# Optimization experiments

Measured on AMD Instinct MI355X. Metric: run time of the kernel, lower is better.

## Reference

```python
import jax, jax.numpy as jnp
import numpy as np

NEG = -1e9  # finite stand-in for -inf (avoids inf-inf NaNs, safe in fp32)


def setup_inputs() -> dict:
    T, V, Lmax, A = 2048, 8192, 8, 64
    rng = np.random.default_rng(0)
    seq = rng.integers(0, A, size=T).astype(np.int32)
    # first A pieces are the single codepoints -> every sequence is segmentable
    piece_lens = np.concatenate([
        np.ones(A, np.int32),
        rng.integers(1, Lmax + 1, size=V - A).astype(np.int32),
    ])
    pieces = rng.integers(0, A, size=(V, Lmax)).astype(np.int32)
    pieces[:A, 0] = np.arange(A)
    logits = rng.standard_normal(V).astype(np.float32)
    m = logits.max()
    log_probs = (logits - m - np.log(np.exp(logits - m).sum())).astype(np.float32)
    return {
        'seq': jnp.asarray(seq),
        'pieces': jnp.asarray(pieces),
        'piece_lens': jnp.asarray(piece_lens),
        'log_probs': jnp.asarray(log_probs),
    }


def reference(seq, pieces, piece_lens, log_probs):
    T = seq.shape[0]
    V, Lmax = pieces.shape
    dt = log_probs.dtype

    # --- match table: match[t, i] = piece i matches sequence at position t ---
    seq_pad = jnp.concatenate([seq, jnp.full((Lmax,), -1, seq.dtype)])
    windows = seq_pad[jnp.arange(T)[:, None] + jnp.arange(Lmax)[None, :]]  # [T, Lmax]
    lmask = jnp.arange(Lmax)[None, :] < piece_lens[:, None]                # [V, Lmax]
    eq = windows[:, None, :] == pieces[None, :, :]                        # [T, V, Lmax]
    fits = (jnp.arange(T)[:, None] + piece_lens[None, :]) <= T            # [T, V]
    match = jnp.all(eq | ~lmask[None, :, :], axis=-1) & fits              # [T, V]
    mlp = jnp.where(match, log_probs[None, :], NEG).astype(dt)            # [T, V]

    # end_logp[t-1, i] = mlp[t - len_i, i]  (piece i ending exactly at t, t=1..T)
    te = jnp.arange(1, T + 1)[:, None]
    src = te - piece_lens[None, :]
    end_logp = jnp.where(src >= 0,
                         mlp[jnp.clip(src, 0, T - 1), jnp.arange(V)[None, :]],
                         NEG)

    # --- forward pass: alpha[t] = logsumexp_i alpha[t - len_i] + log p_i ---
    idx_a = Lmax - piece_lens  # window slot holding alpha[t - len_i]
    def fstep(win, row):
        a_t = jax.nn.logsumexp(win[idx_a] + row)
        return jnp.concatenate([win[1:], a_t[None]]), a_t
    win0 = jnp.full((Lmax,), NEG, dt).at[-1].set(0.0)
    _, alpha_rest = jax.lax.scan(fstep, win0, end_logp)
    alpha = jnp.concatenate([jnp.zeros((1,), dt), alpha_rest])  # [T+1]

    # --- backward pass: beta[t] = logsumexp_i log p_i + beta[t + len_i] ---
    idx_b = piece_lens - 1  # window slot holding beta[t + len_i]
    def bstep(win, row):
        b_t = jax.nn.logsumexp(row + win[idx_b])
        return jnp.concatenate([b_t[None], win[:-1]]), b_t
    winT = jnp.full((Lmax,), NEG, dt).at[0].set(0.0)
    _, beta_rev = jax.lax.scan(bstep, winT, mlp[::-1])
    beta = jnp.concatenate([beta_rev[::-1], jnp.zeros((1,), dt)])  # [T+1]

    # --- posteriors: P[t, i] = exp(alpha[t] + log p_i + beta[t+len_i] - alpha[T]) ---
    norm = alpha[T]
    beta_next = beta[jnp.clip(jnp.arange(T)[:, None] + piece_lens[None, :], 0, T)]
    P = jnp.exp(alpha[:T][:, None] + mlp + beta_next - norm)
    P = jnp.where(match, P, 0.0)
    return jnp.where(norm > NEG / 2, P, jnp.zeros_like(P))
```

## Files before the change

### kernel.cpp

```cpp
#include <hip/hip_runtime.h>
#include <stdint.h>

#define LMAX 8
#define KCH 32
#define NC  64
#define TT  2048
#define LN2D 0.6931471805599453
#define NEGE (-(1<<28))

struct __align__(16) PK { unsigned long long key; float logp; int len; };

__device__ __forceinline__ int fexp(float m) { return ((__float_as_int(m) >> 23) & 0xFF) - 127; }
__device__ __forceinline__ int fexpbits(float m) { return (__float_as_int(m) >> 23) & 0xFF; }
__device__ __forceinline__ float p2(int e) { return __int_as_float((e + 127) << 23); }
__device__ __forceinline__ float p2c(int e) { return (e < -126) ? 0.f : p2(e); }

__global__ void k_prep(const int* __restrict__ seq, const int* __restrict__ pieces,
                       const int* __restrict__ plens, const float* __restrict__ logp,
                       PK* __restrict__ pk, unsigned long long* __restrict__ w64,
                       float* __restrict__ M, int T, int V) {
  int idx = blockIdx.x * blockDim.x + threadIdx.x;
  if (idx < V) {
    const int* pr = pieces + idx * LMAX;
    int len = plens[idx];
    unsigned long long key = 0ull;
    #pragma unroll
    for (int l = 0; l < LMAX; ++l) {
      unsigned long long b = (unsigned long long)(pr[l] & 0xFF);
      if (l < len) key |= b << (8 * l);
    }
    PK o; o.key = key; o.logp = logp[idx]; o.len = len;
    pk[idx] = o;
  } else if (idx < V + T) {
    int t = idx - V;
    unsigned long long w = 0ull;
    #pragma unroll
    for (int l = 0; l < LMAX; ++l) {
      int pos = t + l;
      unsigned long long b = (pos < T) ? (unsigned long long)(seq[pos] & 0xFF) : 0xFFull;
      w |= b << (8 * l);
    }
    w64[t] = w;
  } else if (idx < V + T + T * LMAX) {
    M[idx - V - T] = 0.f;
  }
}

__global__ void k_match(const PK* __restrict__ pk, const unsigned long long* __restrict__ w64,
                        float* __restrict__ M, int T, int V, int tPer) {
  int v = blockIdx.x * blockDim.x + threadIdx.x;
  PK p = pk[v];
  unsigned long long mask = (p.len >= 8) ? ~0ull : ((1ull << (8 * p.len)) - 1ull);
  unsigned long long key = p.key;
  int t0 = blockIdx.y * tPer;
  float prob = -1.f;
  for (int t = t0; t < t0 + tPer; ++t) {
    unsigned long long w = w64[t];
    if (((w ^ key) & mask) == 0ull) {
      if (prob < 0.f) prob = expf(p.logp);
      atomicAdd(&M[t * LMAX + (p.len - 1)], prob);
    }
  }
}

__global__ __launch_bounds__(64, 1) void k_chunks(const float* __restrict__ M,
        float* __restrict__ Wt, int* __restrict__ EWc) {
  int gtid = blockIdx.x * 64 + threadIdx.x;
  int task = gtid >> 3, b = gtid & 7;
  int dir = task >> 6, c = task & 63;
  int base = c * KCH;
  const float4* Mv = (const float4*)M;
  float v[8];
  #pragma unroll
  for (int i = 0; i < 8; ++i) v[i] = (i == b) ? 1.f : 0.f;
  int ec = 0;
  if (dir == 0) {
    float4 ra = Mv[base * 2], rb = Mv[base * 2 + 1];
    for (int kg = 0; kg < 4; ++kg) {
      #pragma unroll
      for (int kk = 0; kk < 8; ++kk) {
        int k = kg * 8 + kk;
        float4 c0 = ra, c1 = rb;
        int nk = (k + 1 < KCH) ? k + 1 : KCH - 1;
        ra = Mv[(base + nk) * 2]; rb = Mv[(base + nk) * 2 + 1];
        float a_ = v[kk & 7];
        v[(kk + 1) & 7] = fmaf(a_, c0.x, v[(kk + 1) & 7]);
        v[(kk + 2) & 7] = fmaf(a_, c0.y, v[(kk + 2) & 7]);
        v[(kk + 3) & 7] = fmaf(a_, c0.z, v[(kk + 3) & 7]);
        v[(kk + 4) & 7] = fmaf(a_, c0.w, v[(kk + 4) & 7]);
        v[(kk + 5) & 7] = fmaf(a_, c1.x, v[(kk + 5) & 7]);
        v[(kk + 6) & 7] = fmaf(a_, c1.y, v[(kk + 6) & 7]);
        v[(kk + 7) & 7] = fmaf(a_, c1.z, v[(kk + 7) & 7]);
        v[kk & 7]       = a_ * c1.w;
        if (kk == 3 || kk == 7) {
          float mx = 0.f;
          #pragma unroll
          for (int i = 0; i < 8; ++i) mx = fmaxf(mx, v[i]);
          if (fexpbits(mx) != 0) {
            int e = fexp(mx); float sc = p2(-e);
            #pragma unroll
            for (int i = 0; i < 8; ++i) v[i] *= sc;
            ec += e;
          }
        }
      }
    }
  } else {
    float4 ra = Mv[(base + KCH - 1) * 2], rb = Mv[(base + KCH - 1) * 2 + 1];
    for (int kg = 0; kg < 4; ++kg) {
      #pragma unroll
      for (int kk = 0; kk < 8; ++kk) {
        int k = kg * 8 + kk;
        float4 c0 = ra, c1 = rb;
        int nk = (k + 1 < KCH) ? k + 1 : KCH - 1;
        int nt = base + KCH - 1 - nk;
        ra = Mv[nt * 2]; rb = Mv[nt * 2 + 1];
        float nb =      c0.x * v[(8  - kk) & 7];
        nb = fmaf(c0.y, v[(9  - kk) & 7], nb);
        nb = fmaf(c0.z, v[(10 - kk) & 7], nb);
        nb = fmaf(c0.w, v[(11 - kk) & 7], nb);
        nb = fmaf(c1.x, v[(12 - kk) & 7], nb);
        nb = fmaf(c1.y, v[(13 - kk) & 7], nb);
        nb = fmaf(c1.z, v[(14 - kk) & 7], nb);
        nb = fmaf(c1.w, v[(15 - kk) & 7], nb);
        v[(7 - kk) & 7] = nb;
        if (kk == 3 || kk == 7) {
          float mx = 0.f;
          #pragma unroll
          for (int i = 0; i < 8; ++i) mx = fmaxf(mx, v[i]);
          if (fexpbits(mx) != 0) {
            int e = fexp(mx); float sc = p2(-e);
            #pragma unroll
            for (int i = 0; i < 8; ++i) v[i] *= sc;
            ec += e;
          }
        }
      }
    }
  }
  float mx = 0.f;
  #pragma unroll
  for (int i = 0; i < 8; ++i) mx = fmaxf(mx, v[i]);
  int ltask = dir * 64 + (dir ? 63 - c : c);
  float* wp = Wt + ltask * 64;
  if (fexpbits(mx) == 0) {
    #pragma unroll
    for (int i = 0; i < 8; ++i) wp[b * 8 + i] = 0.f;
    EWc[ltask * 8 + b] = NEGE;
  } else {
    int e = fexp(mx); float sc = p2(-e);
    #pragma unroll
    for (int i = 0; i < 8; ++i) wp[b * 8 + i] = v[i] * sc;
    EWc[ltask * 8 + b] = ec + e;
  }
}

__global__ __launch_bounds__(128, 1) void k_fin(const float* __restrict__ M,
        const float* __restrict__ Wt, const int* __restrict__ EWc,
        float* __restrict__ Pm, float* __restrict__ aL, float* __restrict__ bL) {
  __shared__ float sWt[128][68];
  __shared__ int   sEW[128 * 8];
  __shared__ int   sEP[128 * 8];
  __shared__ float Gm[16 * 69];
  __shared__ float Sg[16 * 9];
  __shared__ int   EGs[16 * 8];
  __shared__ int   EsB[16];
  __shared__ float sCs[128 * 8];
  __shared__ int   sEacc[128];
  const int tid = threadIdx.x;
  const float4* Mv = (const float4*)M;

  for (int i = tid; i < 128 * 16; i += 128) {
    int task = i >> 4, q = i & 15;
    float4 v4 = ((const float4*)Wt)[i];
    *(float4*)&sWt[task][q * 4] = v4;
  }
  for (int i = tid; i < 1024; i += 128) sEW[i] = EWc[i];
  __syncthreads();

  {
    const int dir = tid >> 6, w = (tid >> 3) & 7, b = tid & 7;
    float v[8];
    #pragma unroll
    for (int i = 0; i < 8; ++i) v[i] = (i == b) ? 1.f : 0.f;
    int ec = 0;
    for (int c = 0; c < 8; ++c) {
      int lc = w * 8 + c, lt = dir * 64 + lc;
      float* pp = Pm + lt * 64 + b * 8;
      #pragma unroll
      for (int i = 0; i < 8; ++i) pp[i] = v[i];
      sEP[lt * 8 + b] = ec;
      const float* wp = &sWt[lt][0];
      int ew[8];
      #pragma unroll
      for (int j = 0; j < 8; ++j) ew[j] = sEW[lt * 8 + j];
      int emax = ew[0];
      #pragma unroll
      for (int j = 1; j < 8; ++j) emax = max(emax, ew[j]);
      float nv[8] = {0, 0, 0, 0, 0, 0, 0, 0};
      #pragma unroll
      for (int j = 0; j < 8; ++j) {
        float tj = v[j] * p2c(ew[j] - emax + 64);
        float4 ca = *(const float4*)(wp + j * 8);
        float4 cb = *(const float4*)(wp + j * 8 + 4);
        nv[0] = fmaf(tj, ca.x, nv[0]); nv[1] = fmaf(tj, ca.y, nv[1]);
        nv[2] = fmaf(tj, ca.z, nv[2]); nv[3] = fmaf(tj, ca.w, nv[3]);
        nv[4] = fmaf(tj, cb.x, nv[4]); nv[5] = fmaf(tj, cb.y, nv[5]);
        nv[6] = fmaf(tj, cb.z, nv[6]); nv[7] = fmaf(tj, cb.w, nv[7]);
      }
      float mx = 0.f;
      #pragma unroll
      for (int i = 0; i < 8; ++i) mx = fmaxf(mx, nv[i]);
      if (fexpbits(mx) == 0) {
        #pragma unroll
        for (int i = 0; i < 8; ++i) v[i] = 0.f;
        ec = NEGE;
      } else {
        int e = fexp(mx); float sc = p2(-e);
        #pragma unroll
        for (int i = 0; i < 8; ++i) v[i] = nv[i] * sc;
        ec = ec + emax + e - 64;
      }
    }
    float* gp = Gm + (dir * 8 + w) * 69 + b * 8;
    #pragma unroll
    for (int i = 0; i < 8; ++i) gp[i] = v[i];
    EGs[(dir * 8 + w) * 8 + b] = ec;
  }
  __syncthreads();

  if (tid < 8 || (tid >= 64 && tid < 72)) {
    const int dir = (tid >= 64) ? 1 : 0, j = tid & 7;
    float s[8];
    #pragma unroll
    for (int i = 0; i < 8; ++i) s[i] = (i == 0) ? 1.f : 0.f;
    int Es = 0;
    for (int w = 0; w < 8; ++w) {
      float sj = s[0];
      #pragma unroll
      for (int i = 1; i < 8; ++i) if (j == i) sj = s[i];
      Sg[(dir * 8 + w) * 9 + j] = sj;
      if (j == 0) EsB[dir * 8 + w] = Es;
      int eg[8];
      #pragma unroll
      for (int i = 0; i < 8; ++i) eg[i] = EGs[(dir * 8 + w) * 8 + i];
      int egmax = eg[0];
      #pragma unroll
      for (int i = 1; i < 8; ++i) egmax = max(egmax, eg[i]);
      int egj = eg[0];
      #pragma unroll
      for (int i = 1; i < 8; ++i) if (j == i) egj = eg[i];
      float tb = sj * p2c(egj - egmax + 64);
      const float* gp = Gm + (dir * 8 + w) * 69 + j * 8;
      float p[8];
      #pragma unroll
      for (int i = 0; i < 8; ++i) p[i] = gp[i] * tb;
      #pragma unroll
      for (int m = 1; m <= 4; m <<= 1)
        #pragma unroll
        for (int i = 0; i < 8; ++i) p[i] += __shfl_xor(p[i], m);
      float mx = 0.f;
      #pragma unroll
      for (int i = 0; i < 8; ++i) mx = fmaxf(mx, p[i]);
      int e = fexp(mx); float sc = p2(-e);
      #pragma unroll
      for (int i = 0; i < 8; ++i) s[i] = p[i] * sc;
      Es += egmax + e - 64;
    }
  }
  __syncthreads();

  {
    const int dir = tid >> 6, lc = tid & 63, w = lc >> 3;
    float sg[8];
    #pragma unroll
    for (int b = 0; b < 8; ++b) sg[b] = Sg[(dir * 8 + w) * 9 + b];
    int Es = EsB[dir * 8 + w];
    int ep[8];
    #pragma unroll
    for (int b = 0; b < 8; ++b) ep[b] = sEP[(dir * 64 + lc) * 8 + b];
    int epmax = ep[0];
    #pragma unroll
    for (int b = 1; b < 8; ++b) epmax = max(epmax, ep[b]);
    float cs[8] = {0, 0, 0, 0, 0, 0, 0, 0};
    #pragma unroll
    for (int b = 0; b < 8; ++b) {
      float coef = sg[b] * p2c(ep[b] - epmax + 64);
      const float* pp = Pm + (dir * 64 + lc) * 64 + b * 8;
      float4 ca = *(const float4*)pp;
      float4 cb = *(const float4*)(pp + 4);
      cs[0] = fmaf(coef, ca.x, cs[0]); cs[1] = fmaf(coef, ca.y, cs[1]);
      cs[2] = fmaf(coef, ca.z, cs[2]); cs[3] = fmaf(coef, ca.w, cs[3]);
      cs[4] = fmaf(coef, cb.x, cs[4]); cs[5] = fmaf(coef, cb.y, cs[5]);
      cs[6] = fmaf(coef, cb.z, cs[6]); cs[7] = fmaf(coef, cb.w, cs[7]);
    }
    float mx = 0.f;
    #pragma unroll
    for (int i = 0; i < 8; ++i) mx = fmaxf(mx, cs[i]);
    int phys = dir ? (63 - lc) : lc;
    float* cp = &sCs[(dir * 64 + phys) * 8];
    if (fexpbits(mx) == 0) {
      #pragma unroll
      for (int i = 0; i < 8; ++i) cp[i] = 0.f;
      sEacc[dir * 64 + phys] = NEGE;
    } else {
      int e = fexp(mx); float sc = p2(-e);
      #pragma unroll
      for (int i = 0; i < 8; ++i) cp[i] = cs[i] * sc;
      sEacc[dir * 64 + phys] = Es + epmax + e - 64;
    }
  }
  __syncthreads();

  {
    const int dir = tid >> 6;
    const int c = tid & 63;
    const int base = c * KCH;
    const float* cp = &sCs[(dir * 64 + c) * 8];
    double st[8];
    #pragma unroll
    for (int i = 0; i < 8; ++i) st[i] = (double)cp[i];
    const double eacc = (double)sEacc[dir * 64 + c];
    if (tid == 0) { aL[0] = 0.f; bL[TT] = 0.f; }
    if (dir == 0) {
      float4 ra = Mv[base * 2], rb = Mv[base * 2 + 1];
      for (int kg = 0; kg < 4; ++kg) {
        #pragma unroll
        for (int kk = 0; kk < 8; ++kk) {
          int k = kg * 8 + kk;
          float4 c0 = ra, c1 = rb;
          int nk = (k + 1 < KCH) ? k + 1 : KCH - 1;
          ra = Mv[(base + nk) * 2]; rb = Mv[(base + nk) * 2 + 1];
          double a_ = st[kk & 7];
          st[(kk + 1) & 7] = fma(a_, (double)c0.x, st[(kk + 1) & 7]);
          st[(kk + 2) & 7] = fma(a_, (double)c0.y, st[(kk + 2) & 7]);
          st[(kk + 3) & 7] = fma(a_, (double)c0.z, st[(kk + 3) & 7]);
          st[(kk + 4) & 7] = fma(a_, (double)c0.w, st[(kk + 4) & 7]);
          st[(kk + 5) & 7] = fma(a_, (double)c1.x, st[(kk + 5) & 7]);
          st[(kk + 6) & 7] = fma(a_, (double)c1.y, st[(kk + 6) & 7]);
          st[(kk + 7) & 7] = fma(a_, (double)c1.z, st[(kk + 7) & 7]);
          st[kk & 7]       = a_ * (double)c1.w;
          double val = st[(kk + 1) & 7];
          long long bits = __double_as_longlong(val);
          int e2 = (int)((bits >> 52) & 0x7ff) - 1023;
          double mant = __longlong_as_double((bits & 0xFFFFFFFFFFFFFLL) | 0x3FF0000000000000LL);
          float lg = log2f((float)mant);
          aL[base + k + 1] = (float)(((double)e2 + eacc + (double)lg) * LN2D);
        }
      }
    } else {
      float4 ra = Mv[(base + KCH - 1) * 2], rb = Mv[(base + KCH - 1) * 2 + 1];
      for (int kg = 0; kg < 4; ++kg) {
        #pragma unroll
        for (int kk = 0; kk < 8; ++kk) {
          int k = kg * 8 + kk;
          int t = base + KCH - 1 - k;
          float4 c0 = ra, c1 = rb;
          int nk = (k + 1 < KCH) ? k + 1 : KCH - 1;
          int nt = base + KCH - 1 - nk;
          ra = Mv[nt * 2]; rb = Mv[nt * 2 + 1];
          double nb =            (double)c0.x * st[(8  - kk) & 7];
          nb = fma((double)c0.y, st[(9  - kk) & 7], nb);
          nb = fma((double)c0.z, st[(10 - kk) & 7], nb);
          nb = fma((double)c0.w, st[(11 - kk) & 7], nb);
          nb = fma((double)c1.x, st[(12 - kk) & 7], nb);
          nb = fma((double)c1.y, st[(13 - kk) & 7], nb);
          nb = fma((double)c1.z, st[(14 - kk) & 7], nb);
          nb = fma((double)c1.w, st[(15 - kk) & 7], nb);
          st[(7 - kk) & 7] = nb;
          long long bits = __double_as_longlong(nb);
          int e2 = (int)((bits >> 52) & 0x7ff) - 1023;
          double mant = __longlong_as_double((bits & 0xFFFFFFFFFFFFFLL) | 0x3FF0000000000000LL);
          float lg = log2f((float)mant);
          bL[t] = (float)(((double)e2 + eacc + (double)lg) * LN2D);
        }
      }
    }
  }
}

__global__ void k_out(const PK* __restrict__ pk, const unsigned long long* __restrict__ w64,
                      const float* __restrict__ aL, const float* __restrict__ bL,
                      float* __restrict__ out, int T, int V, int tPer) {
  int v = blockIdx.x * blockDim.x + threadIdx.x;
  PK p = pk[v];
  unsigned long long mask = (p.len >= 8) ? ~0ull : ((1ull << (8 * p.len)) - 1ull);
  unsigned long long key = p.key;
  float norm = aL[T];
  float base = p.logp - norm;
  int t0 = blockIdx.y * tPer;
  for (int t = t0; t < t0 + tPer; ++t) {
    unsigned long long w = w64[t];
    float val = 0.f;
    if (((w ^ key) & mask) == 0ull)
      val = __expf(aL[t] + base + bL[t + p.len]);
    out[(size_t)t * V + v] = val;
  }
}

extern "C" void kernel_launch(void* const* d_in, const int* in_sizes, int n_in,
                              void* d_out, int out_size, void* d_ws, size_t ws_size,
                              hipStream_t stream) {
  const int* seq    = (const int*)d_in[0];
  const int* pieces = (const int*)d_in[1];
  const int* plens  = (const int*)d_in[2];
  const float* logp = (const float*)d_in[3];
  float* out = (float*)d_out;
  const int T = in_sizes[0];
  const int V = in_sizes[2];

  char* p = (char*)d_ws;
  PK* pk = (PK*)p;                                   p += (size_t)V * sizeof(PK);
  unsigned long long* w64 = (unsigned long long*)p;  p += (size_t)T * 8;
  float* M = (float*)p;                              p += (size_t)T * LMAX * 4;
  float* Wt = (float*)p;                             p += (size_t)128 * 64 * 4;
  int* EWc = (int*)p;                                p += (size_t)128 * 8 * 4;
  float* Pm = (float*)p;                             p += (size_t)128 * 64 * 4;
  float* aL = (float*)p;                             p += 8208;
  float* bL = (float*)p;                             p += 8208;

  int prepN = V + T + T * LMAX;
  k_prep<<<(prepN + 255) / 256, 256, 0, stream>>>(seq, pieces, plens, logp, pk, w64, M, T, V);

  const int tPer2 = 128;
  dim3 g2(V / 256, T / tPer2);
  k_match<<<g2, 256, 0, stream>>>(pk, w64, M, T, V, tPer2);

  k_chunks<<<16, 64, 0, stream>>>(M, Wt, EWc);
  k_fin<<<1, 128, 0, stream>>>(M, Wt, EWc, Pm, aL, bL);

  const int tPer5 = 32;
  dim3 g5(V / 256, T / tPer5);
  k_out<<<g5, 256, 0, stream>>>(pk, w64, aL, bL, out, T, V, tPer5);
}
```

Before: 59.42 us.

## Fuse prep, match and chunk kernels; widen output kernel to float4 stores

Merges the prep, match and per-chunk transfer-matrix kernels into one kernel with one block per 32-position chunk. Matches accumulate in shared memory with shared atomics instead of global atomics, and the chunk scan reads from shared memory. The output kernel now builds piece keys inline and writes four pieces per thread with float4 stores. The aim is to cut launch count and global traffic. The cost is that the fused kernel runs only 64 blocks, each looping over all 8192 pieces, and the chunk-scan stage uses just 16 threads per block.

```diff
diff --git a/kernel.cpp b/kernel.cpp
--- a/kernel.cpp
+++ b/kernel.cpp
@@ -8,150 +8,155 @@
 #define LN2D 0.6931471805599453
 #define NEGE (-(1<<28))
 
-struct __align__(16) PK { unsigned long long key; float logp; int len; };
-
 __device__ __forceinline__ int fexp(float m) { return ((__float_as_int(m) >> 23) & 0xFF) - 127; }
 __device__ __forceinline__ int fexpbits(float m) { return (__float_as_int(m) >> 23) & 0xFF; }
 __device__ __forceinline__ float p2(int e) { return __int_as_float((e + 127) << 23); }
 __device__ __forceinline__ float p2c(int e) { return (e < -126) ? 0.f : p2(e); }
 
-__global__ void k_prep(const int* __restrict__ seq, const int* __restrict__ pieces,
-                       const int* __restrict__ plens, const float* __restrict__ logp,
-                       PK* __restrict__ pk, unsigned long long* __restrict__ w64,
-                       float* __restrict__ M, int T, int V) {
-  int idx = blockIdx.x * blockDim.x + threadIdx.x;
-  if (idx < V) {
-    const int* pr = pieces + idx * LMAX;
-    int len = plens[idx];
+__global__ __launch_bounds__(256, 1) void k_mc(const int* __restrict__ seq,
+        const int* __restrict__ pieces, const int* __restrict__ plens,
+        const float* __restrict__ logp, float* __restrict__ M,
+        float* __restrict__ Wt, int* __restrict__ EWc, int T, int V) {
+  __shared__ int sSeq[40];
+  __shared__ unsigned long long sw[32];
+  __shared__ float sM[32][8];
+  const int tid = threadIdx.x;
+  const int c = blockIdx.x;
+  const int base = c * KCH;
+
+  if (tid < 40) {
+    int pos = base + tid;
+    sSeq[tid] = (pos < T) ? (seq[pos] & 0xFF) : 0xFF;
+  }
+  ((float*)sM)[tid] = 0.f;
+  __syncthreads();
+  if (tid < 32) {
+    unsigned long long w = 0ull;
+    #pragma unroll
+    for (int l = 0; l < LMAX; ++l)
+      w |= (unsigned long long)sSeq[tid + l] << (8 * l);
+    sw[tid] = w;
+  }
+  __syncthreads();
+
+  for (int r = 0; r < 32; ++r) {
+    int v = r * 256 + tid;
+    const int4* pr = (const int4*)(pieces + v * LMAX);
+    int4 pa = pr[0], pb = pr[1];
+    int len = plens[v];
     unsigned long long key = 0ull;
-    #pragma unroll
-    for (int l = 0; l < LMAX; ++l) {
-      unsigned long long b = (unsigned long long)(pr[l] & 0xFF);
-      if (l < len) key |= b << (8 * l);
-    }
-    PK o; o.key = key; o.logp = logp[idx]; o.len = len;
-    pk[idx] = o;
-  } else if (idx < V + T) {
-    int t = idx - V;
-    unsigned long long w = 0ull;
-    #pragma unroll
-    for (int l = 0; l < LMAX; ++l) {
-      int pos = t + l;
-      unsigned long long b = (pos < T) ? (unsigned long long)(seq[pos] & 0xFF) : 0xFFull;
-      w |= b << (8 * l);
-    }
-    w64[t] = w;
-  } else if (idx < V + T + T * LMAX) {
-    M[idx - V - T] = 0.f;
-  }
-}
-
-__global__ void k_match(const PK* __restrict__ pk, const unsigned long long* __restrict__ w64,
-                        float* __restrict__ M, int T, int V, int tPer) {
-  int v = blockIdx.x * blockDim.x + threadIdx.x;
-  PK p = pk[v];
-  unsigned long long mask = (p.len >= 8) ? ~0ull : ((1ull << (8 * p.len)) - 1ull);
-  unsigned long long key = p.key;
-  int t0 = blockIdx.y * tPer;
-  float prob = -1.f;
-  for (int t = t0; t < t0 + tPer; ++t) {
-    unsigned long long w = w64[t];
-    if (((w ^ key) & mask) == 0ull) {
-      if (prob < 0.f) prob = expf(p.logp);
-      atomicAdd(&M[t * LMAX + (p.len - 1)], prob);
-    }
-  }
-}
-
-__global__ __launch_bounds__(64, 1) void k_chunks(const float* __restrict__ M,
-        float* __restrict__ Wt, int* __restrict__ EWc) {
-  int gtid = blockIdx.x * 64 + threadIdx.x;
-  int task = gtid >> 3, b = gtid & 7;
-  int dir = task >> 6, c = task & 63;
-  int base = c * KCH;
-  const float4* Mv = (const float4*)M;
-  float v[8];
-  #pragma unroll
-  for (int i = 0; i < 8; ++i) v[i] = (i == b) ? 1.f : 0.f;
-  int ec = 0;
-  if (dir == 0) {
-    float4 ra = Mv[base * 2], rb = Mv[base * 2 + 1];
-    for (int kg = 0; kg < 4; ++kg) {
-      #pragma unroll
-      for (int kk = 0; kk < 8; ++kk) {
-        int k = kg * 8 + kk;
-        float4 c0 = ra, c1 = rb;
-        int nk = (k + 1 < KCH) ? k + 1 : KCH - 1;
-        ra = Mv[(base + nk) * 2]; rb = Mv[(base + nk) * 2 + 1];
-        float a_ = v[kk & 7];
-        v[(kk + 1) & 7] = fmaf(a_, c0.x, v[(kk + 1) & 7]);
-        v[(kk + 2) & 7] = fmaf(a_, c0.y, v[(kk + 2) & 7]);
-        v[(kk + 3) & 7] = fmaf(a_, c0.z, v[(kk + 3) & 7]);
-        v[(kk + 4) & 7] = fmaf(a_, c0.w, v[(kk + 4) & 7]);
-        v[(kk + 5) & 7] = fmaf(a_, c1.x, v[(kk + 5) & 7]);
-        v[(kk + 6) & 7] = fmaf(a_, c1.y, v[(kk + 6) & 7]);
-        v[(kk + 7) & 7] = fmaf(a_, c1.z, v[(kk + 7) & 7]);
-        v[kk & 7]       = a_ * c1.w;
-        if (kk == 3 || kk == 7) {
-          float mx = 0.f;
-          #pragma unroll
-          for (int i = 0; i < 8; ++i) mx = fmaxf(mx, v[i]);
-          if (fexpbits(mx) != 0) {
-            int e = fexp(mx); float sc = p2(-e);
+    {
+      unsigned long long b0 = (unsigned long long)(pa.x & 0xFF);
+      unsigned long long b1 = (unsigned long long)(pa.y & 0xFF);
+      unsigned long long b2 = (unsigned long long)(pa.z & 0xFF);
+      unsigned long long b3 = (unsigned long long)(pa.w & 0xFF);
+      unsigned long long b4 = (unsigned long long)(pb.x & 0xFF);
+      unsigned long long b5 = (unsigned long long)(pb.y & 0xFF);
+      unsigned long long b6 = (unsigned long long)(pb.z & 0xFF);
+      unsigned long long b7 = (unsigned long long)(pb.w & 0xFF);
+      if (0 < len) key |= b0;
+      if (1 < len) key |= b1 << 8;
+      if (2 < len) key |= b2 << 16;
+      if (3 < len) key |= b3 << 24;
+      if (4 < len) key |= b4 << 32;
+      if (5 < len) key |= b5 << 40;
+      if (6 < len) key |= b6 << 48;
+      if (7 < len) key |= b7 << 56;
+    }
+    unsigned long long mask = (len >= 8) ? ~0ull : ((1ull << (8 * len)) - 1ull);
+    float prob = -1.f;
+    for (int t = 0; t < 32; ++t) {
+      if (((sw[t] ^ key) & mask) == 0ull) {
+        if (prob < 0.f) prob = expf(logp[v]);
+        atomicAdd(&sM[t][len - 1], prob);
+      }
+    }
+  }
+  __syncthreads();
+
+  if (tid < 64) ((float4*)M)[c * 64 + tid] = ((float4*)sM)[tid];
+
+  if (tid < 16) {
+    const int dir = tid >> 3, b = tid & 7;
+    float v[8];
+    #pragma unroll
+    for (int i = 0; i < 8; ++i) v[i] = (i == b) ? 1.f : 0.f;
+    int ec = 0;
+    if (dir == 0) {
+      for (int kg = 0; kg < 4; ++kg) {
+        #pragma unroll
+        for (int kk = 0; kk < 8; ++kk) {
+          int k = kg * 8 + kk;
+          float4 c0 = *(const float4*)&sM[k][0];
+          float4 c1 = *(const float4*)&sM[k][4];
+          float a_ = v[kk & 7];
+          v[(kk + 1) & 7] = fmaf(a_, c0.x, v[(kk + 1) & 7]);
+          v[(kk + 2) & 7] = fmaf(a_, c0.y, v[(kk + 2) & 7]);
+          v[(kk + 3) & 7] = fmaf(a_, c0.z, v[(kk + 3) & 7]);
+          v[(kk + 4) & 7] = fmaf(a_, c0.w, v[(kk + 4) & 7]);
+          v[(kk + 5) & 7] = fmaf(a_, c1.x, v[(kk + 5) & 7]);
+          v[(kk + 6) & 7] = fmaf(a_, c1.y, v[(kk + 6) & 7]);
+          v[(kk + 7) & 7] = fmaf(a_, c1.z, v[(kk + 7) & 7]);
+          v[kk & 7]       = a_ * c1.w;
+          if (kk == 3 || kk == 7) {
+            float mx = 0.f;
             #pragma unroll
-            for (int i = 0; i < 8; ++i) v[i] *= sc;
-            ec += e;
+            for (int i = 0; i < 8; ++i) mx = fmaxf(mx, v[i]);
+            if (fexpbits(mx) != 0) {
+              int e = fexp(mx); float sc = p2(-e);
+              #pragma unroll
+              for (int i = 0; i < 8; ++i) v[i] *= sc;
+              ec += e;
+            }
           }
         }
       }
-    }
-  } else {
-    float4 ra = Mv[(base + KCH - 1) * 2], rb = Mv[(base + KCH - 1) * 2 + 1];
-    for (int kg = 0; kg < 4; ++kg) {
-      #pragma unroll
-      for (int kk = 0; kk < 8; ++kk) {
-        int k = kg * 8 + kk;
-        float4 c0 = ra, c1 = rb;
-        int nk = (k + 1 < KCH) ? k + 1 : KCH - 1;
-        int nt = base + KCH - 1 - nk;
-        ra = Mv[nt * 2]; rb = Mv[nt * 2 + 1];
-        float nb =      c0.x * v[(8  - kk) & 7];
-        nb = fmaf(c0.y, v[(9  - kk) & 7], nb);
-        nb = fmaf(c0.z, v[(10 - kk) & 7], nb);
-        nb = fmaf(c0.w, v[(11 - kk) & 7], nb);
-        nb = fmaf(c1.x, v[(12 - kk) & 7], nb);
-        nb = fmaf(c1.y, v[(13 - kk) & 7], nb);
-        nb = fmaf(c1.z, v[(14 - kk) & 7], nb);
-        nb = fmaf(c1.w, v[(15 - kk) & 7], nb);
-        v[(7 - kk) & 7] = nb;
-        if (kk == 3 || kk == 7) {
-          float mx = 0.f;
-          #pragma unroll
-          for (int i = 0; i < 8; ++i) mx = fmaxf(mx, v[i]);
-          if (fexpbits(mx) != 0) {
-            int e = fexp(mx); float sc = p2(-e);
+    } else {
+      for (int kg = 0; kg < 4; ++kg) {
+        #pragma unroll
+        for (int kk = 0; kk < 8; ++kk) {
+          int k = kg * 8 + kk;
+          int r = KCH - 1 - k;
+          float4 c0 = *(const float4*)&sM[r][0];
+          float4 c1 = *(const float4*)&sM[r][4];
+          float nb =      c0.x * v[(8  - kk) & 7];
+          nb = fmaf(c0.y, v[(9  - kk) & 7], nb);
+          nb = fmaf(c0.z, v[(10 - kk) & 7], nb);
+          nb = fmaf(c0.w, v[(11 - kk) & 7], nb);
+          nb = fmaf(c1.x, v[(12 - kk) & 7], nb);
+          nb = fmaf(c1.y, v[(13 - kk) & 7], nb);
+          nb = fmaf(c1.z, v[(14 - kk) & 7], nb);
+          nb = fmaf(c1.w, v[(15 - kk) & 7], nb);
+          v[(7 - kk) & 7] = nb;
+          if (kk == 3 || kk == 7) {
+            float mx = 0.f;
             #pragma unroll
-            for (int i = 0; i < 8; ++i) v[i] *= sc;
-            ec += e;
+            for (int i = 0; i < 8; ++i) mx = fmaxf(mx, v[i]);
+            if (fexpbits(mx) != 0) {
+              int e = fexp(mx); float sc = p2(-e);
+              #pragma unroll
+              for (int i = 0; i < 8; ++i) v[i] *= sc;
+              ec += e;
+            }
           }
         }
       }
     }
-  }
-  float mx = 0.f;
-  #pragma unroll
-  for (int i = 0; i < 8; ++i) mx = fmaxf(mx, v[i]);
-  int ltask = dir * 64 + (dir ? 63 - c : c);
-  float* wp = Wt + ltask * 64;
-  if (fexpbits(mx) == 0) {
-    #pragma unroll
-    for (int i = 0; i < 8; ++i) wp[b * 8 + i] = 0.f;
-    EWc[ltask * 8 + b] = NEGE;
-  } else {
-    int e = fexp(mx); float sc = p2(-e);
-    #pragma unroll
-    for (int i = 0; i < 8; ++i) wp[b * 8 + i] = v[i] * sc;
-    EWc[ltask * 8 + b] = ec + e;
+    float mx = 0.f;
+    #pragma unroll
+    for (int i = 0; i < 8; ++i) mx = fmaxf(mx, v[i]);
+    int ltask = dir * 64 + (dir ? 63 - c : c);
+    float* wp = Wt + ltask * 64;
+    if (fexpbits(mx) == 0) {
+      #pragma unroll
+      for (int i = 0; i < 8; ++i) wp[b * 8 + i] = 0.f;
+      EWc[ltask * 8 + b] = NEGE;
+    } else {
+      int e = fexp(mx); float sc = p2(-e);
+      #pragma unroll
+      for (int i = 0; i < 8; ++i) wp[b * 8 + i] = v[i] * sc;
+      EWc[ltask * 8 + b] = ec + e;
+    }
   }
 }
 
@@ -379,22 +384,64 @@
   }
 }
 
-__global__ void k_out(const PK* __restrict__ pk, const unsigned long long* __restrict__ w64,
-                      const float* __restrict__ aL, const float* __restrict__ bL,
-                      float* __restrict__ out, int T, int V, int tPer) {
-  int v = blockIdx.x * blockDim.x + threadIdx.x;
-  PK p = pk[v];
-  unsigned long long mask = (p.len >= 8) ? ~0ull : ((1ull << (8 * p.len)) - 1ull);
-  unsigned long long key = p.key;
+__global__ __launch_bounds__(256) void k_out(const int* __restrict__ seq,
+        const int* __restrict__ pieces, const int* __restrict__ plens,
+        const float* __restrict__ logp, const float* __restrict__ aL,
+        const float* __restrict__ bL, float* __restrict__ out, int T, int V) {
+  __shared__ int sSeq[40];
+  __shared__ unsigned long long sw[32];
+  const int tid = threadIdx.x;
+  const int t0 = blockIdx.y * 32;
+  const int v0 = blockIdx.x * 1024 + tid * 4;
+  if (tid < 40) {
+    int pos = t0 + tid;
+    sSeq[tid] = (pos < T) ? (seq[pos] & 0xFF) : 0xFF;
+  }
+  __syncthreads();
+  if (tid < 32) {
+    unsigned long long w = 0ull;
+    #pragma unroll
+    for (int l = 0; l < LMAX; ++l)
+      w |= (unsigned long long)sSeq[tid + l] << (8 * l);
+    sw[tid] = w;
+  }
+  __syncthreads();
+
   float norm = aL[T];
-  float base = p.logp - norm;
-  int t0 = blockIdx.y * tPer;
-  for (int t = t0; t < t0 + tPer; ++t) {
-    unsigned long long w = w64[t];
-    float val = 0.f;
-    if (((w ^ key) & mask) == 0ull)
-      val = __expf(aL[t] + base + bL[t + p.len]);
-    out[(size_t)t * V + v] = val;
+  unsigned long long key[4], mask[4];
+  int len[4];
+  float lpb[4];
+  #pragma unroll
+  for (int j = 0; j < 4; ++j) {
+    int v = v0 + j;
+    const int4* pr = (const int4*)(pieces + v * LMAX);
+    int4 pa = pr[0], pb = pr[1];
+    int ln = plens[v];
+    unsigned long long k_ = 0ull;
+    if (0 < ln) k_ |= (unsigned long long)(pa.x & 0xFF);
+    if (1 < ln) k_ |= (unsigned long long)(pa.y & 0xFF) << 8;
+    if (2 < ln) k_ |= (unsigned long long)(pa.z & 0xFF) << 16;
+    if (3 < ln) k_ |= (unsigned long long)(pa.w & 0xFF) << 24;
+    if (4 < ln) k_ |= (unsigned long long)(pb.x & 0xFF) << 32;
+    if (5 < ln) k_ |= (unsigned long long)(pb.y & 0xFF) << 40;
+    if (6 < ln) k_ |= (unsigned long long)(pb.z & 0xFF) << 48;
+    if (7 < ln) k_ |= (unsigned long long)(pb.w & 0xFF) << 56;
+    key[j] = k_;
+    mask[j] = (ln >= 8) ? ~0ull : ((1ull << (8 * ln)) - 1ull);
+    len[j] = ln;
+    lpb[j] = logp[v] - norm;
+  }
+
+  for (int tt = 0; tt < 32; ++tt) {
+    int t = t0 + tt;
+    unsigned long long w = sw[tt];
+    float al = aL[t];
+    float4 o = make_float4(0.f, 0.f, 0.f, 0.f);
+    if (((w ^ key[0]) & mask[0]) == 0ull) o.x = __expf(al + lpb[0] + bL[t + len[0]]);
+    if (((w ^ key[1]) & mask[1]) == 0ull) o.y = __expf(al + lpb[1] + bL[t + len[1]]);
+    if (((w ^ key[2]) & mask[2]) == 0ull) o.z = __expf(al + lpb[2] + bL[t + len[2]]);
+    if (((w ^ key[3]) & mask[3]) == 0ull) o.w = __expf(al + lpb[3] + bL[t + len[3]]);
+    *(float4*)&out[(size_t)t * V + v0] = o;
   }
 }
 
@@ -410,26 +457,15 @@
   const int V = in_sizes[2];
 
   char* p = (char*)d_ws;
-  PK* pk = (PK*)p;                                   p += (size_t)V * sizeof(PK);
-  unsigned long long* w64 = (unsigned long long*)p;  p += (size_t)T * 8;
-  float* M = (float*)p;                              p += (size_t)T * LMAX * 4;
-  float* Wt = (float*)p;                             p += (size_t)128 * 64 * 4;
-  int* EWc = (int*)p;                                p += (size_t)128 * 8 * 4;
-  float* Pm = (float*)p;                             p += (size_t)128 * 64 * 4;
-  float* aL = (float*)p;                             p += 8208;
-  float* bL = (float*)p;                             p += 8208;
-
-  int prepN = V + T + T * LMAX;
-  k_prep<<<(prepN + 255) / 256, 256, 0, stream>>>(seq, pieces, plens, logp, pk, w64, M, T, V);
-
-  const int tPer2 = 128;
-  dim3 g2(V / 256, T / tPer2);
-  k_match<<<g2, 256, 0, stream>>>(pk, w64, M, T, V, tPer2);
-
-  k_chunks<<<16, 64, 0, stream>>>(M, Wt, EWc);
+  float* M = (float*)p;    p += (size_t)T * LMAX * 4;
+  float* Wt = (float*)p;   p += (size_t)128 * 64 * 4;
+  int* EWc = (int*)p;      p += (size_t)128 * 8 * 4;
+  float* Pm = (float*)p;   p += (size_t)128 * 64 * 4;
+  float* aL = (float*)p;   p += 8208;
+  float* bL = (float*)p;   p += 8208;
+
+  k_mc<<<NC, 256, 0, stream>>>(seq, pieces, plens, logp, M, Wt, EWc, T, V);
   k_fin<<<1, 128, 0, stream>>>(M, Wt, EWc, Pm, aL, bL);
-
-  const int tPer5 = 32;
-  dim3 g5(V / 256, T / tPer5);
-  k_out<<<g5, 256, 0, stream>>>(pk, w64, aL, bL, out, T, V, tPer5);
+  dim3 g3(V / 1024, T / 32);
+  k_out<<<g3, 256, 0, stream>>>(seq, pieces, plens, logp, aL, bL, out, T, V);
 }
```

Result: slower. 111.3 us (+87.3%).
